# Performance work log

Measured on AMD Instinct MI355X. Metric: run time of the kernel, lower is better.

The kernel has to match this reference:

```python
import jax, jax.numpy as jnp
import numpy as np

B, T, D, H = 2, 1024, 1024, 16
WINDOW = 32
KSZ = 2 * WINDOW + 1
MAXG = 32


def setup_inputs() -> dict:
    key = jax.random.key(0)
    ks = jax.random.split(key, 5)
    s = 0.02
    x = jax.random.normal(ks[0], (B, T, D), jnp.float32)
    Wq = jax.random.normal(ks[1], (D, D), jnp.float32) * s
    Wk = jax.random.normal(ks[2], (D, D), jnp.float32) * s
    Wv = jax.random.normal(ks[3], (D, D), jnp.float32) * s
    Wo = jax.random.normal(ks[4], (D, D), jnp.float32) * s
    # global tokens: one every T//MAXG positions (same for every batch row)
    global_mask = jnp.tile((jnp.arange(T) % (T // MAXG) == 0)[None, :], (B, 1))
    return {"x": x, "global_mask": global_mask, "Wq": Wq, "Wk": Wk,
            "Wv": Wv, "Wo": Wo, "maxG": MAXG}


def reference(x, global_mask, Wq, Wk, Wv, Wo, maxG):
    Bb, Tt, Dm = x.shape
    dh = Dm // H
    scale = dh ** -0.5

    def proj(W):
        return (x @ W.T).reshape(Bb, Tt, H, dh).transpose(0, 2, 1, 3)  # (B,H,T,dh)

    q, k, v = proj(Wq), proj(Wk), proj(Wv)

    # sliding windows via zero-padded gather (== F.unfold with padding=WINDOW)
    widx = jnp.arange(Tt)[:, None] + jnp.arange(KSZ)[None, :]  # index into padded axis

    def windows(t):
        tp = jnp.pad(t, ((0, 0), (0, 0), (WINDOW, WINDOW), (0, 0)))
        return tp[:, :, widx, :]  # (B,H,T,KSZ,dh)

    Kw, Vw = windows(k), windows(v)
    scores_local = jnp.einsum('bhtd,bhtwd->bhtw', q, Kw) * scale

    # pack global-token indices (stable argsort puts True positions first, in order)
    order = jnp.argsort(jnp.logical_not(global_mask), axis=1, stable=True)
    gidx = order[:, :maxG]                                   # (B,maxG)
    gvalid = jnp.take_along_axis(global_mask, gidx, axis=1)  # (B,maxG) bool
    gather_b = jax.vmap(lambda arr, i: arr[:, i, :])         # (H,T,dh),(maxG,)->(H,maxG,dh)
    Kg = gather_b(k, gidx) * gvalid[:, None, :, None]
    Vg = gather_b(v, gidx) * gvalid[:, None, :, None]

    scores_global = jnp.einsum('bhtd,bhgd->bhtg', q, Kg) * scale
    scores_global = jnp.where(gvalid[:, None, None, :], scores_global, -1e9)

    attn = jax.nn.softmax(jnp.concatenate([scores_local, scores_global], axis=-1), axis=-1)
    wl, wg = attn[..., :KSZ], attn[..., KSZ:]
    ctx = (jnp.einsum('bhtw,bhtwd->bhtd', wl, Vw)
           + jnp.einsum('bhtg,bhgd->bhtd', wg, Vg))
    out = ctx.transpose(0, 2, 1, 3).reshape(Bb, Tt, Dm) @ Wo.T

    # ---- debug full attention map (vectorized replica of the per-token loop) ----
    t = jnp.arange(Tt)
    left = jnp.maximum(0, t - WINDOW)
    win_len = jnp.minimum(Tt, t + WINDOW + 1) - left           # (T,)
    valid_w = jnp.arange(KSZ)[None, :] < win_len[:, None]      # (T,KSZ)
    s_loc = jnp.where(valid_w[None, None], scores_local, -jnp.inf)
    attn_d = jax.nn.softmax(jnp.concatenate([s_loc, scores_global], axis=-1), axis=-1)
    wl_d = attn_d[..., :KSZ] * valid_w[None, None]             # (B,H,T,KSZ)
    wg_d = attn_d[..., KSZ:] * gvalid[:, None, None, :]        # (B,H,T,maxG)
    cols = jnp.minimum(left[:, None] + jnp.arange(KSZ)[None, :], Tt - 1)  # (T,KSZ)
    rows = jnp.broadcast_to(t[:, None], (Tt, KSZ))
    full_attn = jnp.zeros((Bb, H, Tt, Tt), x.dtype)
    full_attn = full_attn.at[:, :, rows, cols].add(wl_d)
    full_attn = jax.vmap(lambda fa, w, gi: fa.at[:, :, gi].add(w))(full_attn, wg_d, gidx)
    return out, full_attn
```

## Files before the change

kernel.cpp:

```cpp
#include <hip/hip_runtime.h>

#define T_   1024
#define B_   2
#define H_   16
#define DH   64
#define D_   1024
#define WND  32
#define KSZ  65
#define NG   32

typedef float f32x4 __attribute__((ext_vector_type(4)));
typedef __bf16 bf16x8 __attribute__((ext_vector_type(8)));
typedef __bf16 bf16x4 __attribute__((ext_vector_type(4)));
typedef unsigned short u16x4 __attribute__((ext_vector_type(4)));

__device__ __forceinline__ unsigned short f2bf(float f) {
  unsigned u = __float_as_uint(f);
  return (unsigned short)((u + 0x7fffu + ((u >> 16) & 1u)) >> 16);
}

__global__ __launch_bounds__(256) void cvt_kernel(const float* __restrict__ x,
    const float* __restrict__ wq, const float* __restrict__ wk,
    const float* __restrict__ wv, const float* __restrict__ wo,
    unsigned short* __restrict__ dst,
    const int* __restrict__ mask, int* __restrict__ gidxo, float* __restrict__ gvalo) {
  if (blockIdx.x == 6144) {
    if (threadIdx.x < 128) {
      int b = threadIdx.x >> 6, lane = threadIdx.x & 63;
      const int* mb = mask + b * T_;
      unsigned long long lanemask = (1ull << lane) - 1ull;
      int base = 0;
      for (int c = 0; c < 16 && base < NG; ++c) {
        int t = c * 64 + lane;
        bool m = mb[t] != 0;
        unsigned long long bal = __ballot(m);
        int rank = __popcll(bal & lanemask);
        if (m && base + rank < NG) { gidxo[b*NG+base+rank] = t; gvalo[b*NG+base+rank] = 1.f; }
        base += __popcll(bal);
      }
      if (base < NG) {
        for (int c = 0; c < 16 && base < NG; ++c) {
          int t = c * 64 + lane;
          bool m = mb[t] == 0;
          unsigned long long bal = __ballot(m);
          int rank = __popcll(bal & lanemask);
          if (m && base + rank < NG) { gidxo[b*NG+base+rank] = t; gvalo[b*NG+base+rank] = 0.f; }
          base += __popcll(bal);
        }
      }
    }
    return;
  }
  int idx = (blockIdx.x * 256 + threadIdx.x) * 4;
  int r = idx >> 20;
  const float* src; int off;
  if (r < 2)       { src = x;  off = idx; }
  else if (r == 2) { src = wq; off = idx - 2 * 1048576; }
  else if (r == 3) { src = wk; off = idx - 3 * 1048576; }
  else if (r == 4) { src = wv; off = idx - 4 * 1048576; }
  else             { src = wo; off = idx - 5 * 1048576; }
  f32x4 v = *(const f32x4*)(src + off);
  u16x4 o;
  o.x = f2bf(v[0]); o.y = f2bf(v[1]); o.z = f2bf(v[2]); o.w = f2bf(v[3]);
  *(u16x4*)(dst + idx) = o;
}

template<int MODE, int BM>
__global__ __launch_bounds__(256) void gemm128(const unsigned short* __restrict__ A,
    const unsigned short* __restrict__ B0, const unsigned short* __restrict__ B1,
    const unsigned short* __restrict__ B2,
    void* __restrict__ C0v, void* __restrict__ C1v, void* __restrict__ C2v) {
  constexpr int K = 1024;
  constexpr int FM = BM / 32;
  constexpr int ACH = BM * 8 / 256;
  constexpr int WM = BM / 2;
  __shared__ __attribute__((aligned(16))) unsigned short SMEM[BM * 64 + 128 * 64];
  unsigned short* As = SMEM;
  unsigned short* Bs = SMEM + BM * 64;

  int m0 = blockIdx.x * BM, n0 = blockIdx.y * 128;
  int zz = (MODE == 0) ? blockIdx.z : 0;
  const unsigned short* Bb = (MODE == 0) ? (zz == 0 ? B0 : (zz == 1 ? B1 : B2)) : B0;

  int tid = threadIdx.x;
  int w = tid >> 6, l = tid & 63;
  int wr = w >> 1, wc = w & 1;
  int lr = l & 15, kg = l >> 4;

  f32x4 acc[FM][4] = {};

  for (int kt = 0; kt < K; kt += 64) {
    __syncthreads();
#pragma unroll
    for (int i = 0; i < ACH; ++i) {
      int ci = tid + 256 * i;
      int row = ci >> 3, c8 = ci & 7;
      *(bf16x8*)&As[row * 64 + ((c8 ^ (row & 7)) * 8)] =
          *(const bf16x8*)&A[(size_t)(m0 + row) * K + kt + c8 * 8];
    }
#pragma unroll
    for (int i = 0; i < 4; ++i) {
      int ci = tid + 256 * i;
      int row = ci >> 3, c8 = ci & 7;
      *(bf16x8*)&Bs[row * 64 + ((c8 ^ (row & 7)) * 8)] =
          *(const bf16x8*)&Bb[(size_t)(n0 + row) * K + kt + c8 * 8];
    }
    __syncthreads();
#pragma unroll
    for (int kk = 0; kk < 2; ++kk) {
      int c8 = kk * 4 + kg;
      bf16x8 af[FM], bfr[4];
#pragma unroll
      for (int mi = 0; mi < FM; ++mi) {
        int row = wr * WM + mi * 16 + lr;
        af[mi] = *(bf16x8*)&As[row * 64 + ((c8 ^ (row & 7)) * 8)];
      }
#pragma unroll
      for (int ni = 0; ni < 4; ++ni) {
        int row = wc * 64 + ni * 16 + lr;
        bfr[ni] = *(bf16x8*)&Bs[row * 64 + ((c8 ^ (row & 7)) * 8)];
      }
#pragma unroll
      for (int mi = 0; mi < FM; ++mi)
#pragma unroll
        for (int ni = 0; ni < 4; ++ni)
          acc[mi][ni] = __builtin_amdgcn_mfma_f32_16x16x32_bf16(af[mi], bfr[ni], acc[mi][ni], 0, 0, 0);
    }
  }

  if (MODE == 1) {
    float* C = (float*)C0v;
#pragma unroll
    for (int mi = 0; mi < FM; ++mi)
#pragma unroll
      for (int ni = 0; ni < 4; ++ni) {
        int mbase = m0 + wr * WM + mi * 16 + (l >> 4) * 4;
        int n = n0 + wc * 64 + ni * 16 + lr;
#pragma unroll
        for (int r = 0; r < 4; ++r)
          C[(size_t)(mbase + r) * 1024 + n] = acc[mi][ni][r];
      }
  } else if (zz < 2) {
    unsigned short* C = (unsigned short*)(zz == 0 ? C0v : C1v);
#pragma unroll
    for (int mi = 0; mi < FM; ++mi)
#pragma unroll
      for (int ni = 0; ni < 4; ++ni) {
        int mbase = m0 + wr * WM + mi * 16 + (l >> 4) * 4;
        int n = n0 + wc * 64 + ni * 16 + lr;
#pragma unroll
        for (int r = 0; r < 4; ++r) {
          __bf16 v = (__bf16)acc[mi][ni][r];
          C[(size_t)(mbase + r) * 1024 + n] = *(unsigned short*)&v;
        }
      }
  } else {
    constexpr int RS = BM * 2;
    constexpr int TCH = BM / 8;
    constexpr int NIT = 128 * TCH / 256;
    __syncthreads();
    char* Tb = (char*)SMEM;
#pragma unroll
    for (int mi = 0; mi < FM; ++mi)
#pragma unroll
      for (int ni = 0; ni < 4; ++ni) {
        int mb2 = wr * WM + mi * 16 + (l >> 4) * 4;
        int nl = wc * 64 + ni * 16 + lr;
        bf16x4 pk;
        pk[0] = (__bf16)acc[mi][ni][0]; pk[1] = (__bf16)acc[mi][ni][1];
        pk[2] = (__bf16)acc[mi][ni][2]; pk[3] = (__bf16)acc[mi][ni][3];
        *(bf16x4*)(Tb + ((nl * RS + mb2 * 2) ^ ((nl & 7) << 4))) = pk;
      }
    __syncthreads();
    unsigned short* C = (unsigned short*)C2v;
    int bb = m0 >> 10, tbase = m0 & 1023;
#pragma unroll
    for (int it = 0; it < NIT; ++it) {
      int ci = tid + 256 * it;
      int dl = ci / TCH, tc = ci % TCH;
      bf16x8 v = *(bf16x8*)(Tb + ((dl * RS + tc * 16) ^ ((dl & 7) << 4)));
      int n = n0 + dl, hh = n >> 6, dd = n & 63;
      *(bf16x8*)&C[((size_t)(bb * H_ + hh) * DH + dd) * T_ + tbase + tc * 8] = v;
    }
  }
}

__global__ __launch_bounds__(512, 4) void attn_kernel(
    const unsigned short* __restrict__ qg, const unsigned short* __restrict__ kg_,
    const unsigned short* __restrict__ vg,
    const int* __restrict__ gidx_g, const float* __restrict__ gval_g,
    unsigned short* __restrict__ ctxb, float* __restrict__ fa) {
  int tid = threadIdx.x;
  int t0 = blockIdx.x * 32;
  int h = blockIdx.y, b = blockIdx.z;
  int lane = tid & 63, wv = tid >> 6;

  __shared__ __attribute__((aligned(16))) unsigned short QbL[32 * 64];
  __shared__ __attribute__((aligned(16))) unsigned short KbL[128 * 64];
  __shared__ __attribute__((aligned(16))) unsigned short VtL[64 * 128];
  __shared__ __attribute__((aligned(16))) unsigned short WbL[32 * 128];
  __shared__ __attribute__((aligned(16))) float Sf[32][132];
  __shared__ float m_out_s[32], invdo_s[32], rowfac_s[32];
  __shared__ int   gidx_s[32];
  __shared__ float gval_s[32];

  if (tid < 32) { gidx_s[tid] = gidx_g[b * NG + tid]; gval_s[tid] = gval_g[b * NG + tid]; }
  ((unsigned long long*)WbL)[tid] = 0ull;
  ((unsigned long long*)WbL)[tid + 512] = 0ull;
  __syncthreads();

  const unsigned short* qbh = qg + (size_t)(b * T_ + t0) * D_ + h * DH;
  const unsigned short* kbh = kg_ + (size_t)(b * T_) * D_ + h * DH;
  const unsigned short* vbh = vg + (size_t)(b * H_ + h) * DH * T_;

  if (tid < 256) {
    int r = tid >> 3, c8 = tid & 7;
    bf16x8 v = *(const bf16x8*)(qbh + (size_t)r * D_ + c8 * 8);
    *(bf16x8*)((char*)QbL + ((r * 128 + c8 * 16) ^ ((r & 7) << 4))) = v;
  }
#pragma unroll
  for (int it = 0; it < 2; ++it) {
    int fi = tid + it * 512;
    int r = fi >> 3, c8 = fi & 7;
    int col; bool valid;
    if (r < 96) { col = t0 - 32 + r; valid = (col >= 0 && col < T_); }
    else { int g = r - 96; valid = gval_s[g] > 0.f; col = valid ? gidx_s[g] : 0; }
    bf16x8 v = {};
    if (valid) v = *(const bf16x8*)(kbh + (size_t)col * D_ + c8 * 8);
    *(bf16x8*)((char*)KbL + ((r * 128 + c8 * 16) ^ ((r & 7) << 4))) = v;
  }
#pragma unroll
  for (int it = 0; it < 2; ++it) {
    int fi = tid + it * 512;
    if (fi < 768) {
      int d = fi / 12, rc = fi % 12;
      int cb = t0 - 32 + rc * 8;
      bf16x8 v = {};
      if (cb >= 0 && cb < T_) v = *(const bf16x8*)(vbh + d * T_ + cb);
      *(bf16x8*)((char*)VtL + ((d * 256 + rc * 16) ^ ((d & 7) << 4))) = v;
    }
  }
#pragma unroll
  for (int it = 0; it < 4; ++it) {
    int fi = tid + it * 512;
    int d = fi >> 5, g = fi & 31;
    unsigned short v = 0;
    if (gval_s[g] > 0.f) v = vbh[d * T_ + gidx_s[g]];
    *(unsigned short*)((char*)VtL + ((d * 256 + (96 + g) * 2) ^ ((d & 7) << 4))) = v;
  }
  __syncthreads();

  {
    int mt = wv & 1, nq = wv >> 1;
    int lrr = lane & 15, kgl = lane >> 4;
    int arow = mt * 16 + lrr;
    f32x4 acc0 = {}, acc1 = {};
#pragma unroll
    for (int s = 0; s < 2; ++s) {
      int c = s * 4 + kgl;
      bf16x8 a = *(bf16x8*)((char*)QbL + ((arow * 128 + c * 16) ^ ((arow & 7) << 4)));
      int br0 = nq * 32 + lrr, br1 = nq * 32 + 16 + lrr;
      bf16x8 b0 = *(bf16x8*)((char*)KbL + ((br0 * 128 + c * 16) ^ ((br0 & 7) << 4)));
      bf16x8 b1 = *(bf16x8*)((char*)KbL + ((br1 * 128 + c * 16) ^ ((br1 & 7) << 4)));
      acc0 = __builtin_amdgcn_mfma_f32_16x16x32_bf16(a, b0, acc0, 0, 0, 0);
      acc1 = __builtin_amdgcn_mfma_f32_16x16x32_bf16(a, b1, acc1, 0, 0, 0);
    }
    int orow = mt * 16 + (lane >> 4) * 4;
#pragma unroll
    for (int i = 0; i < 4; ++i) {
      Sf[orow + i][nq * 32 + lrr] = acc0[i] * 0.125f;
      Sf[orow + i][nq * 32 + 16 + lrr] = acc1[i] * 0.125f;
    }
  }
  __syncthreads();

  {
    int r = tid >> 4, lg = tid & 15;
    int t_abs = t0 + r;
    int left = (t_abs - WND > 0) ? (t_abs - WND) : 0;
    int tmp = t_abs + WND + 1; if (tmp > T_) tmp = T_;
    int wl = tmp - left;
    float sv[8]; bool vld[8], vdd[8];
#pragma unroll
    for (int ii = 0; ii < 8; ++ii) {
      int c = lg + ii * 16;
      bool loc = (c >= r && c <= r + 64);
      bool glob = (c >= 96);
      float s = Sf[r][c];
      if (glob && !(gval_s[c - 96] > 0.f)) s = -1e9f;
      vld[ii] = loc || glob;
      vdd[ii] = loc ? ((c - r) < wl) : glob;
      sv[ii] = s;
    }
    float mo = -1e30f, md = -1e30f;
#pragma unroll
    for (int ii = 0; ii < 8; ++ii) {
      if (vld[ii]) mo = fmaxf(mo, sv[ii]);
      if (vdd[ii]) md = fmaxf(md, sv[ii]);
    }
#pragma unroll
    for (int o = 1; o < 16; o <<= 1) {
      mo = fmaxf(mo, __shfl_xor(mo, o, 16));
      md = fmaxf(md, __shfl_xor(md, o, 16));
    }
    float eo = 0.f, ed = 0.f;
#pragma unroll
    for (int ii = 0; ii < 8; ++ii) {
      if (vld[ii]) eo += __expf(sv[ii] - mo);
      if (vdd[ii]) ed += __expf(sv[ii] - md);
    }
#pragma unroll
    for (int o = 1; o < 16; o <<= 1) {
      eo += __shfl_xor(eo, o, 16);
      ed += __shfl_xor(ed, o, 16);
    }
    if (lg == 0) {
      m_out_s[r] = mo;
      invdo_s[r] = 1.f / eo;
      rowfac_s[r] = (eo / ed) * __expf(mo - md);
    }
  }
  __syncthreads();

  for (int idx = tid; idx < 32 * 97; idx += 512) {
    int t = idx / 97;
    int j = idx - t * 97;
    int cc = (j < KSZ) ? (t + j) : (j + 31);
    float s = Sf[t][cc];
    float wgt = __expf(s - m_out_s[t]) * invdo_s[t];
    Sf[t][cc] = wgt;
    *(unsigned short*)((char*)WbL + ((t * 256 + cc * 2) ^ ((t & 7) << 4))) = f2bf(wgt);
  }
  __syncthreads();

  {
    int mt = wv >> 1, nt = wv & 1;
    int lrr = lane & 15, kgl = lane >> 4;
    int arow = mt * 16 + lrr;
    int brow = nt * 16 + lrr;
    f32x4 acc = {};
#pragma unroll
    for (int s = 0; s < 4; ++s) {
      int c = s * 4 + kgl;
      bf16x8 a = *(bf16x8*)((char*)VtL + ((arow * 256 + c * 16) ^ ((arow & 7) << 4)));
      bf16x8 bb = *(bf16x8*)((char*)WbL + ((brow * 256 + c * 16) ^ ((brow & 7) << 4)));
      acc = __builtin_amdgcn_mfma_f32_16x16x32_bf16(a, bb, acc, 0, 0, 0);
    }
    int t = nt * 16 + lrr;
    int dbase = mt * 16 + (lane >> 4) * 4;
    u16x4 st;
    st.x = f2bf(acc[0]); st.y = f2bf(acc[1]); st.z = f2bf(acc[2]); st.w = f2bf(acc[3]);
    *(u16x4*)(ctxb + ((size_t)(b * T_ + t0 + t)) * D_ + h * DH + dbase) = st;
  }

  {
    int rp = tid >> 8;
    int c0 = (tid & 255) * 4;
    unsigned gm = 0;
#pragma unroll
    for (int g = 0; g < NG; ++g) {
      int gc = gidx_s[g];
      if (gval_s[g] > 0.f && gc >= c0 && gc < c0 + 4) gm |= (1u << g);
    }
#pragma unroll 2
    for (int rr = 0; rr < 16; ++rr) {
      int r = rr * 2 + rp;
      int t_abs = t0 + r;
      int left = (t_abs - WND > 0) ? (t_abs - WND) : 0;
      int tmp = t_abs + WND + 1; if (tmp > T_) tmp = T_;
      int wl = tmp - left;
      float rf = rowfac_s[r];
      f32x4 o = {0.f, 0.f, 0.f, 0.f};
      int jj0 = c0 - left;
      if (jj0 > -4 && jj0 < wl) {
#pragma unroll
        for (int e = 0; e < 4; ++e) {
          int jj = jj0 + e;
          if (jj >= 0 && jj < wl) o[e] = Sf[r][r + jj] * rf;
        }
      }
      if (gm) {
        unsigned mm = gm;
        while (mm) {
          int g = __ffs(mm) - 1; mm &= mm - 1;
          o[gidx_s[g] - c0] += Sf[r][96 + g] * rf;
        }
      }
      float* dst = fa + (((size_t)(b * H_ + h) * T_) + t_abs) * T_ + c0;
      *(f32x4*)dst = o;
    }
  }
}

extern "C" void kernel_launch(void* const* d_in, const int* in_sizes, int n_in,
                              void* d_out, int out_size, void* d_ws, size_t ws_size,
                              hipStream_t stream) {
  const float* x   = (const float*)d_in[0];
  const int* gmask = (const int*)d_in[1];
  const float* wq  = (const float*)d_in[2];
  const float* wk  = (const float*)d_in[3];
  const float* wv  = (const float*)d_in[4];
  const float* wo  = (const float*)d_in[5];

  unsigned short* arena = (unsigned short*)d_ws;
  unsigned short* xb  = arena;
  unsigned short* wqb = arena + 2 * 1048576;
  unsigned short* wkb = arena + 3 * 1048576;
  unsigned short* wvb = arena + 4 * 1048576;
  unsigned short* wob = arena + 5 * 1048576;
  unsigned short* qb   = arena + 6 * 1048576;
  unsigned short* kb   = arena + 8 * 1048576;
  unsigned short* vtb  = arena + 10 * 1048576;
  unsigned short* ctxb = arena + 12 * 1048576;
  int*   gidx = (int*)(arena + 14 * 1048576);
  float* gval = (float*)(gidx + 64);

  float* outp = (float*)d_out;
  float* fa   = outp + 2097152;

  cvt_kernel<<<dim3(6145), dim3(256), 0, stream>>>(x, wq, wk, wv, wo, xb, gmask, gidx, gval);
  gemm128<0, 64><<<dim3(32, 8, 3), dim3(256), 0, stream>>>(xb, wqb, wkb, wvb, qb, kb, vtb);
  attn_kernel<<<dim3(32, 16, 2), dim3(512), 0, stream>>>(qb, kb, vtb, gidx, gval, ctxb, fa);
  gemm128<1, 64><<<dim3(32, 8, 1), dim3(256), 0, stream>>>(ctxb, wob, wob, wob, outp, outp, outp);
}
```

Baseline: 93.10 us.

## Fuse Q/K/V projections into one GEMM kernel sharing the A tile

Replaces the three-way gridded QKV GEMM with a single 512-thread kernel that loads each x tile once and multiplies it against the Wq, Wk and Wv tiles together, keeping three accumulator sets. This removes the redundant A-tile global loads across the z dimension. The trade-off is that the grid drops from 768 blocks to 256, and the kernel uses more LDS and more registers per block, so the GPU may be less fully occupied. The output GEMM is split into its own specialized kernel with unchanged logic.

Measured after the change: 96.77 us. +3.9%, slower.

```diff
diff --git a/kernel.cpp b/kernel.cpp
--- a/kernel.cpp
+++ b/kernel.cpp
@@ -65,34 +65,130 @@
   *(u16x4*)(dst + idx) = o;
 }
 
-template<int MODE, int BM>
-__global__ __launch_bounds__(256) void gemm128(const unsigned short* __restrict__ A,
+__global__ __launch_bounds__(512, 2) void qkv_fused(const unsigned short* __restrict__ A,
     const unsigned short* __restrict__ B0, const unsigned short* __restrict__ B1,
     const unsigned short* __restrict__ B2,
-    void* __restrict__ C0v, void* __restrict__ C1v, void* __restrict__ C2v) {
+    unsigned short* __restrict__ Cq, unsigned short* __restrict__ Ck,
+    unsigned short* __restrict__ Cv) {
   constexpr int K = 1024;
-  constexpr int FM = BM / 32;
-  constexpr int ACH = BM * 8 / 256;
-  constexpr int WM = BM / 2;
-  __shared__ __attribute__((aligned(16))) unsigned short SMEM[BM * 64 + 128 * 64];
+  __shared__ __attribute__((aligned(16))) unsigned short SMEM[4096 + 3 * 8192];
   unsigned short* As = SMEM;
-  unsigned short* Bs = SMEM + BM * 64;
-
-  int m0 = blockIdx.x * BM, n0 = blockIdx.y * 128;
-  int zz = (MODE == 0) ? blockIdx.z : 0;
-  const unsigned short* Bb = (MODE == 0) ? (zz == 0 ? B0 : (zz == 1 ? B1 : B2)) : B0;
-
+  unsigned short* Bs = SMEM + 4096;
+
+  int m0 = blockIdx.x * 64, n0 = blockIdx.y * 128;
+  int tid = threadIdx.x;
+  int w = tid >> 6, l = tid & 63;
+  int wr = w >> 2, wcq = w & 3;
+  int lr = l & 15, kg = l >> 4;
+
+  f32x4 acc[3][2][2] = {};
+
+  for (int kt = 0; kt < K; kt += 64) {
+    __syncthreads();
+    {
+      int row = tid >> 3, c8 = tid & 7;
+      *(bf16x8*)&As[row * 64 + ((c8 ^ (row & 7)) * 8)] =
+          *(const bf16x8*)&A[(size_t)(m0 + row) * K + kt + c8 * 8];
+    }
+#pragma unroll
+    for (int z = 0; z < 3; ++z) {
+      const unsigned short* Bz = (z == 0) ? B0 : (z == 1 ? B1 : B2);
+#pragma unroll
+      for (int i = 0; i < 2; ++i) {
+        int ci = tid + i * 512;
+        int row = ci >> 3, c8 = ci & 7;
+        *(bf16x8*)&Bs[z * 8192 + row * 64 + ((c8 ^ (row & 7)) * 8)] =
+            *(const bf16x8*)&Bz[(size_t)(n0 + row) * K + kt + c8 * 8];
+      }
+    }
+    __syncthreads();
+#pragma unroll
+    for (int kk = 0; kk < 2; ++kk) {
+      int c8 = kk * 4 + kg;
+      bf16x8 af[2], bfz[3][2];
+#pragma unroll
+      for (int mi = 0; mi < 2; ++mi) {
+        int row = wr * 32 + mi * 16 + lr;
+        af[mi] = *(bf16x8*)&As[row * 64 + ((c8 ^ (row & 7)) * 8)];
+      }
+#pragma unroll
+      for (int z = 0; z < 3; ++z)
+#pragma unroll
+        for (int ni = 0; ni < 2; ++ni) {
+          int row = wcq * 32 + ni * 16 + lr;
+          bfz[z][ni] = *(bf16x8*)&Bs[z * 8192 + row * 64 + ((c8 ^ (row & 7)) * 8)];
+        }
+#pragma unroll
+      for (int z = 0; z < 3; ++z)
+#pragma unroll
+        for (int mi = 0; mi < 2; ++mi)
+#pragma unroll
+          for (int ni = 0; ni < 2; ++ni)
+            acc[z][mi][ni] = __builtin_amdgcn_mfma_f32_16x16x32_bf16(af[mi], bfz[z][ni], acc[z][mi][ni], 0, 0, 0);
+    }
+  }
+
+#pragma unroll
+  for (int z = 0; z < 2; ++z) {
+    unsigned short* C = z ? Ck : Cq;
+#pragma unroll
+    for (int mi = 0; mi < 2; ++mi)
+#pragma unroll
+      for (int ni = 0; ni < 2; ++ni) {
+        int mbase = m0 + wr * 32 + mi * 16 + (l >> 4) * 4;
+        int n = n0 + wcq * 32 + ni * 16 + lr;
+#pragma unroll
+        for (int r = 0; r < 4; ++r) {
+          __bf16 v = (__bf16)acc[z][mi][ni][r];
+          C[(size_t)(mbase + r) * 1024 + n] = *(unsigned short*)&v;
+        }
+      }
+  }
+
+  __syncthreads();
+  char* Tb = (char*)SMEM;
+#pragma unroll
+  for (int mi = 0; mi < 2; ++mi)
+#pragma unroll
+    for (int ni = 0; ni < 2; ++ni) {
+      int mb2 = wr * 32 + mi * 16 + (l >> 4) * 4;
+      int nl = wcq * 32 + ni * 16 + lr;
+      bf16x4 pk;
+      pk[0] = (__bf16)acc[2][mi][ni][0]; pk[1] = (__bf16)acc[2][mi][ni][1];
+      pk[2] = (__bf16)acc[2][mi][ni][2]; pk[3] = (__bf16)acc[2][mi][ni][3];
+      *(bf16x4*)(Tb + ((nl * 128 + mb2 * 2) ^ ((nl & 7) << 4))) = pk;
+    }
+  __syncthreads();
+  int bb = m0 >> 10, tbase = m0 & 1023;
+#pragma unroll
+  for (int it = 0; it < 2; ++it) {
+    int ci = tid + it * 512;
+    int dl = ci >> 3, tc = ci & 7;
+    bf16x8 v = *(bf16x8*)(Tb + ((dl * 128 + tc * 16) ^ ((dl & 7) << 4)));
+    int n = n0 + dl, hh = n >> 6, dd = n & 63;
+    *(bf16x8*)&Cv[((size_t)(bb * H_ + hh) * DH + dd) * T_ + tbase + tc * 8] = v;
+  }
+}
+
+__global__ __launch_bounds__(256) void out_gemm(const unsigned short* __restrict__ A,
+    const unsigned short* __restrict__ Bw, float* __restrict__ C) {
+  constexpr int K = 1024;
+  __shared__ __attribute__((aligned(16))) unsigned short SMEM[64 * 64 + 128 * 64];
+  unsigned short* As = SMEM;
+  unsigned short* Bs = SMEM + 64 * 64;
+
+  int m0 = blockIdx.x * 64, n0 = blockIdx.y * 128;
   int tid = threadIdx.x;
   int w = tid >> 6, l = tid & 63;
   int wr = w >> 1, wc = w & 1;
   int lr = l & 15, kg = l >> 4;
 
-  f32x4 acc[FM][4] = {};
+  f32x4 acc[2][4] = {};
 
   for (int kt = 0; kt < K; kt += 64) {
     __syncthreads();
 #pragma unroll
-    for (int i = 0; i < ACH; ++i) {
+    for (int i = 0; i < 2; ++i) {
       int ci = tid + 256 * i;
       int row = ci >> 3, c8 = ci & 7;
       *(bf16x8*)&As[row * 64 + ((c8 ^ (row & 7)) * 8)] =
@@ -103,16 +199,16 @@
       int ci = tid + 256 * i;
       int row = ci >> 3, c8 = ci & 7;
       *(bf16x8*)&Bs[row * 64 + ((c8 ^ (row & 7)) * 8)] =
-          *(const bf16x8*)&Bb[(size_t)(n0 + row) * K + kt + c8 * 8];
+          *(const bf16x8*)&Bw[(size_t)(n0 + row) * K + kt + c8 * 8];
     }
     __syncthreads();
 #pragma unroll
     for (int kk = 0; kk < 2; ++kk) {
       int c8 = kk * 4 + kg;
-      bf16x8 af[FM], bfr[4];
-#pragma unroll
-      for (int mi = 0; mi < FM; ++mi) {
-        int row = wr * WM + mi * 16 + lr;
+      bf16x8 af[2], bfr[4];
+#pragma unroll
+      for (int mi = 0; mi < 2; ++mi) {
+        int row = wr * 32 + mi * 16 + lr;
         af[mi] = *(bf16x8*)&As[row * 64 + ((c8 ^ (row & 7)) * 8)];
       }
 #pragma unroll
@@ -121,68 +217,23 @@
         bfr[ni] = *(bf16x8*)&Bs[row * 64 + ((c8 ^ (row & 7)) * 8)];
       }
 #pragma unroll
-      for (int mi = 0; mi < FM; ++mi)
+      for (int mi = 0; mi < 2; ++mi)
 #pragma unroll
         for (int ni = 0; ni < 4; ++ni)
           acc[mi][ni] = __builtin_amdgcn_mfma_f32_16x16x32_bf16(af[mi], bfr[ni], acc[mi][ni], 0, 0, 0);
     }
   }
 
-  if (MODE == 1) {
-    float* C = (float*)C0v;
-#pragma unroll
-    for (int mi = 0; mi < FM; ++mi)
-#pragma unroll
-      for (int ni = 0; ni < 4; ++ni) {
-        int mbase = m0 + wr * WM + mi * 16 + (l >> 4) * 4;
-        int n = n0 + wc * 64 + ni * 16 + lr;
-#pragma unroll
-        for (int r = 0; r < 4; ++r)
-          C[(size_t)(mbase + r) * 1024 + n] = acc[mi][ni][r];
-      }
-  } else if (zz < 2) {
-    unsigned short* C = (unsigned short*)(zz == 0 ? C0v : C1v);
-#pragma unroll
-    for (int mi = 0; mi < FM; ++mi)
-#pragma unroll
-      for (int ni = 0; ni < 4; ++ni) {
-        int mbase = m0 + wr * WM + mi * 16 + (l >> 4) * 4;
-        int n = n0 + wc * 64 + ni * 16 + lr;
-#pragma unroll
-        for (int r = 0; r < 4; ++r) {
-          __bf16 v = (__bf16)acc[mi][ni][r];
-          C[(size_t)(mbase + r) * 1024 + n] = *(unsigned short*)&v;
-        }
-      }
-  } else {
-    constexpr int RS = BM * 2;
-    constexpr int TCH = BM / 8;
-    constexpr int NIT = 128 * TCH / 256;
-    __syncthreads();
-    char* Tb = (char*)SMEM;
-#pragma unroll
-    for (int mi = 0; mi < FM; ++mi)
-#pragma unroll
-      for (int ni = 0; ni < 4; ++ni) {
-        int mb2 = wr * WM + mi * 16 + (l >> 4) * 4;
-        int nl = wc * 64 + ni * 16 + lr;
-        bf16x4 pk;
-        pk[0] = (__bf16)acc[mi][ni][0]; pk[1] = (__bf16)acc[mi][ni][1];
-        pk[2] = (__bf16)acc[mi][ni][2]; pk[3] = (__bf16)acc[mi][ni][3];
-        *(bf16x4*)(Tb + ((nl * RS + mb2 * 2) ^ ((nl & 7) << 4))) = pk;
-      }
-    __syncthreads();
-    unsigned short* C = (unsigned short*)C2v;
-    int bb = m0 >> 10, tbase = m0 & 1023;
-#pragma unroll
-    for (int it = 0; it < NIT; ++it) {
-      int ci = tid + 256 * it;
-      int dl = ci / TCH, tc = ci % TCH;
-      bf16x8 v = *(bf16x8*)(Tb + ((dl * RS + tc * 16) ^ ((dl & 7) << 4)));
-      int n = n0 + dl, hh = n >> 6, dd = n & 63;
-      *(bf16x8*)&C[((size_t)(bb * H_ + hh) * DH + dd) * T_ + tbase + tc * 8] = v;
-    }
-  }
+#pragma unroll
+  for (int mi = 0; mi < 2; ++mi)
+#pragma unroll
+    for (int ni = 0; ni < 4; ++ni) {
+      int mbase = m0 + wr * 32 + mi * 16 + (l >> 4) * 4;
+      int n = n0 + wc * 64 + ni * 16 + lr;
+#pragma unroll
+      for (int r = 0; r < 4; ++r)
+        C[(size_t)(mbase + r) * 1024 + n] = acc[mi][ni][r];
+    }
 }
 
 __global__ __launch_bounds__(512, 4) void attn_kernel(
@@ -419,7 +470,7 @@
   float* fa   = outp + 2097152;
 
   cvt_kernel<<<dim3(6145), dim3(256), 0, stream>>>(x, wq, wk, wv, wo, xb, gmask, gidx, gval);
-  gemm128<0, 64><<<dim3(32, 8, 3), dim3(256), 0, stream>>>(xb, wqb, wkb, wvb, qb, kb, vtb);
+  qkv_fused<<<dim3(32, 8), dim3(512), 0, stream>>>(xb, wqb, wkb, wvb, qb, kb, vtb);
   attn_kernel<<<dim3(32, 16, 2), dim3(512), 0, stream>>>(qb, kb, vtb, gidx, gval, ctxb, fa);
-  gemm128<1, 64><<<dim3(32, 8, 1), dim3(256), 0, stream>>>(ctxb, wob, wob, wob, outp, outp, outp);
-}
+  out_gemm<<<dim3(32, 8), dim3(256), 0, stream>>>(ctxb, wob, outp);
+}
```
